# Kernel tuning notes

Hardware: AMD Instinct MI355X
Metric: run time of the kernel (lower is better)

## Reference

```python
import jax, jax.numpy as jnp
import numpy as np

NUM_ANTENNAS = 16
D = 0.5
WAVELENGTH = 1.0
RHO = 0.8


def setup_inputs() -> dict:
    key = jax.random.key(0)
    k = jax.random.split(key, 5)
    return {
        "W": jax.random.normal(k[0], (2_000_000, 2 * NUM_ANTENNAS), dtype=jnp.float32),
        "Hc_real": jax.random.normal(k[1], (4, 8, NUM_ANTENNAS), dtype=jnp.float32),
        "Hc_imag": jax.random.normal(k[2], (4, 8, NUM_ANTENNAS), dtype=jnp.float32),
        "Hs_real": jax.random.normal(k[3], (4, 4, NUM_ANTENNAS), dtype=jnp.float32),
        "Hs_imag": jax.random.normal(k[4], (4, 4, NUM_ANTENNAS), dtype=jnp.float32),
    }


def _estimate_angles(h_real, h_imag):
    """Vectorized version of the per-(b,t) phase-unwrap + OLS slope fit.

    h_real/h_imag: [B, T, N] -> angles [B, T] in degrees.
    """
    n = jnp.arange(NUM_ANTENNAS, dtype=h_real.dtype)
    phases = jnp.arctan2(h_imag, h_real)                      # torch.angle
    pd = jnp.diff(phases, axis=-1)
    pd = (pd + jnp.pi) % (2.0 * jnp.pi) - jnp.pi              # wrap to (-pi, pi]
    zeros = jnp.zeros(phases.shape[:-1] + (1,), phases.dtype)
    unwrapped = jnp.concatenate([zeros, jnp.cumsum(pd, axis=-1)], axis=-1)  # [B,T,N]
    # OLS slope of unwrapped vs n (closed form of solve(XtX, XtY) with X=[n,1])
    n_c = n - n.mean()
    slope = (unwrapped * n_c).sum(-1) / (n_c * n_c).sum()     # [B,T]
    sin_theta = jnp.clip(slope * WAVELENGTH / (2.0 * jnp.pi * D), -1.0, 1.0)
    return -jnp.rad2deg(jnp.arcsin(sin_theta))


def _steering_phase(angles_deg):
    # phase[t, n] = 2*pi*d*n*sin(theta_t)/wavelength  -> [T, N]
    n = jnp.arange(NUM_ANTENNAS, dtype=angles_deg.dtype)
    s = jnp.sin(jnp.deg2rad(angles_deg))
    return 2.0 * jnp.pi * D * s[:, None] * n[None, :] / WAVELENGTH


def reference(W, Hc_real, Hc_imag, Hs_real, Hs_imag):
    user_angles = _estimate_angles(Hc_real, Hc_imag)[0]       # [Tc]
    target_angles = _estimate_angles(Hs_real, Hs_imag)[0]     # [Ts]

    Wr = W[:, :NUM_ANTENNAS]
    Wi = W[:, NUM_ANTENNAS:]

    def gains(phase):  # |w_cplx @ conj(sv).T|, all-real math
        c = jnp.cos(phase)  # [T, N]
        s = jnp.sin(phase)
        re = Wr @ c.T + Wi @ s.T  # [B, T]
        im = Wi @ c.T - Wr @ s.T
        return jnp.sqrt(re * re + im * im)

    user_gains = gains(_steering_phase(user_angles))          # [B, Tc]
    target_gains = gains(_steering_phase(target_angles))      # [B, Ts]

    min_user_gain = user_gains.min(axis=1)
    sum_user_gain = user_gains.sum(axis=1)
    avg_target_gain = target_gains.mean(axis=1)

    comm_loss = -RHO * 2.5 * (min_user_gain + 0.1 * sum_user_gain)
    sens_loss = -(1.0 - RHO) * avg_target_gain
    return jnp.mean(comm_loss + sens_loss)
```

## Files before the change

kernel.cpp:

```cpp
#include <hip/hip_runtime.h>
#include <math.h>

#define NA 16
#define NBEAM 12
#define NUSER 8

#define ACC_OFFSET 1536

__global__ void mtl_angles_kernel(const float* __restrict__ Hc_r, const float* __restrict__ Hc_i,
                                  const float* __restrict__ Hs_r, const float* __restrict__ Hs_i,
                                  float* __restrict__ table, double* __restrict__ acc,
                                  unsigned* __restrict__ done) {
    int t = threadIdx.x;
    if (t == 0) { *acc = 0.0; *done = 0u; }
    if (t >= NBEAM) return;

    const float* re;
    const float* im;
    if (t < NUSER) { re = Hc_r + t * NA;           im = Hc_i + t * NA; }
    else           { re = Hs_r + (t - NUSER) * NA; im = Hs_i + (t - NUSER) * NA; }

    const float PI_F   = 3.14159265358979323846f;
    const float TWO_PI = 6.28318530717958647692f;

    float ph[NA];
    #pragma unroll
    for (int n = 0; n < NA; ++n) ph[n] = atan2f(im[n], re[n]);

    float unw = 0.f, dotsum = 0.f;
    #pragma unroll
    for (int n = 1; n < NA; ++n) {
        float pd = ph[n] - ph[n - 1];
        float x  = pd + PI_F;
        float m  = fmodf(x, TWO_PI);
        if (m < 0.f) m += TWO_PI;
        pd = m - PI_F;
        unw += pd;
        dotsum += unw * ((float)n - 7.5f);
    }
    float slope = dotsum / 340.0f;
    float sin_theta = slope / PI_F;
    sin_theta = fminf(1.0f, fmaxf(-1.0f, sin_theta));
    float st = -sin_theta;

    #pragma unroll
    for (int n = 0; n < NA; ++n) {
        float phase = PI_F * st * (float)n;
        table[t * 2 * NA + n]      = cosf(phase);
        table[t * 2 * NA + NA + n] = sinf(phase);
    }
}

__device__ __forceinline__ float dot4(float4 a, float4 b) {
    return a.x * b.x + a.y * b.y + a.z * b.z + a.w * b.w;
}

__device__ __forceinline__ void load_lds16(const float* g, float* l) {
    __builtin_amdgcn_global_load_lds(
        (const __attribute__((address_space(1))) void*)g,
        (__attribute__((address_space(3))) void*)l, 16, 0, 0);
}

__device__ __forceinline__ float row_loss(const float4* w, const float* tbs) {
    float minU = 3.4e38f, sumU = 0.f, sumT = 0.f;
    #pragma unroll 1
    for (int j = 0; j < NBEAM; ++j) {
        const float4* tc = (const float4*)(tbs + j * 32);
        float re = 0.f, im = 0.f;
        #pragma unroll
        for (int q = 0; q < 4; ++q) {
            float4 c = tc[q], s = tc[q + 4];
            float4 wr = w[q], wi = w[q + 4];
            re += dot4(wr, c) + dot4(wi, s);
            im += dot4(wi, c) - dot4(wr, s);
        }
        float g = sqrtf(re * re + im * im);
        if (j < NUSER) { minU = fminf(minU, g); sumU += g; }
        else           { sumT += g; }
    }
    return -2.0f * (minU + 0.1f * sumU) - 0.05f * sumT;
}

__global__ __launch_bounds__(256, 4) void mtl_gains_kernel(const float* __restrict__ W,
                                                           const float* __restrict__ table,
                                                           double* __restrict__ acc,
                                                           unsigned* __restrict__ done,
                                                           float* __restrict__ out, int rows) {
    __shared__ float sh[4 * 2 * 1024];
    __shared__ float tbs[NBEAM * 2 * NA];
    __shared__ float wsum[4];

    const int t = threadIdx.x;
    for (int i = t; i < NBEAM * 2 * NA; i += blockDim.x) tbs[i] = table[i];
    __syncthreads();

    const int wid  = t >> 6;
    const int lane = t & 63;
    float* buf0 = sh + wid * 2048;
    float* buf1 = buf0 + 1024;

    const int sq      = (lane & 7) ^ ((lane >> 3) & 7);
    const int src_off = (lane >> 3) * 32 + sq * 4;

    const int ntiles = rows >> 5;
    const int nwaves = gridDim.x * 4;
    const int gw     = blockIdx.x * 4 + wid;
    const int cnt    = ntiles / nwaves;
    const int rem    = ntiles % nwaves;
    const int t0     = gw * cnt + (gw < rem ? gw : rem);
    const int t1     = t0 + cnt + (gw < rem ? 1 : 0);

    const int h      = lane >> 5;
    const int row    = lane & 31;
    const int jbase  = h * 6;
    const float* tb  = tbs + jbase * 2 * NA;

    float local = 0.f;

    if (t0 < t1) {
        {
            const float* src = W + (size_t)t0 * 1024 + src_off;
            #pragma unroll
            for (int k = 0; k < 4; ++k) load_lds16(src + k * 256, buf0 + k * 256);
        }
        #pragma unroll 1
        for (int tt = t0; tt < t1; ++tt) {
            float* cur = ((tt - t0) & 1) ? buf1 : buf0;
            float* nxt = ((tt - t0) & 1) ? buf0 : buf1;
            if (tt + 1 < t1) {
                const float* src = W + (size_t)(tt + 1) * 1024 + src_off;
                #pragma unroll
                for (int k = 0; k < 4; ++k) load_lds16(src + k * 256, nxt + k * 256);
                asm volatile("s_waitcnt vmcnt(4)" ::: "memory");
            } else {
                asm volatile("s_waitcnt vmcnt(0)" ::: "memory");
            }

            const float* myrow = cur + row * 32;
            float4 w[8];
            #pragma unroll
            for (int q = 0; q < 8; ++q) {
                int s = q ^ (row & 7);
                w[q] = *(const float4*)(myrow + s * 4);
            }

            float minU = 3.4e38f, sumU = 0.f, sumT = 0.f;
            #pragma unroll 1
            for (int jj = 0; jj < 6; ++jj) {
                const float4* tc = (const float4*)(tb + jj * 32);
                float re = 0.f, im = 0.f;
                #pragma unroll
                for (int q = 0; q < 4; ++q) {
                    float4 c = tc[q], s = tc[q + 4];
                    float4 wr = w[q], wi = w[q + 4];
                    re += dot4(wr, c) + dot4(wi, s);
                    im += dot4(wi, c) - dot4(wr, s);
                }
                float g = sqrtf(re * re + im * im);
                bool isU = (jbase + jj) < NUSER;
                minU = isU ? fminf(minU, g) : minU;
                sumU += isU ? g : 0.f;
                sumT += isU ? 0.f : g;
            }
            minU = fminf(minU, __shfl_xor(minU, 32));
            sumU += __shfl_xor(sumU, 32);
            sumT += __shfl_xor(sumT, 32);
            local += 0.5f * (-2.0f * (minU + 0.1f * sumU) - 0.05f * sumT);
        }
    }

    int tailbase = ntiles << 5;
    if (blockIdx.x == 0) {
        int r = tailbase + t;
        if (r < rows) {
            const float4* wp = (const float4*)(W + (size_t)r * 32);
            float4 w[8];
            #pragma unroll
            for (int i = 0; i < 8; ++i) w[i] = wp[i];
            local += row_loss(w, tbs);
        }
    }

    #pragma unroll
    for (int off = 32; off > 0; off >>= 1) local += __shfl_down(local, off);
    if (lane == 0) wsum[wid] = local;
    __syncthreads();
    if (t == 0) {
        float b = wsum[0] + wsum[1] + wsum[2] + wsum[3];
        atomicAdd(acc, (double)b);
        __threadfence();
        unsigned prev = atomicAdd(done, 1u);
        if (prev == gridDim.x - 1) {
            double total = atomicAdd(acc, 0.0);
            out[0] = (float)(total / (double)rows);
        }
    }
}

extern "C" void kernel_launch(void* const* d_in, const int* in_sizes, int n_in,
                              void* d_out, int out_size, void* d_ws, size_t ws_size,
                              hipStream_t stream) {
    const float* W    = (const float*)d_in[0];
    const float* Hc_r = (const float*)d_in[1];
    const float* Hc_i = (const float*)d_in[2];
    const float* Hs_r = (const float*)d_in[3];
    const float* Hs_i = (const float*)d_in[4];
    float* out = (float*)d_out;

    int rows = in_sizes[0] / (2 * NA);
    float*    table = (float*)d_ws;
    double*   acc   = (double*)((char*)d_ws + ACC_OFFSET);
    unsigned* done  = (unsigned*)((char*)d_ws + ACC_OFFSET + 8);

    mtl_angles_kernel<<<1, 64, 0, stream>>>(Hc_r, Hc_i, Hs_r, Hs_i, table, acc, done);

    mtl_gains_kernel<<<1024, 256, 0, stream>>>(W, table, acc, done, out, rows);
}
```

Baseline: 408.4 us.

## Replace last-block completion counter with separate finalize kernel and split beam loops

Removes the threadfence and done-counter atomic that let the last block compute the final mean, and launches a tiny finalize kernel instead. The per-row beam loop is split into a user loop and a target loop so the per-iteration user/target select logic disappears. Launch bounds are expressed through an explicit waves-per-EU attribute. The extra kernel launch adds a small fixed cost in exchange for less per-block synchronisation.

```diff
diff --git a/kernel.cpp b/kernel.cpp
--- a/kernel.cpp
+++ b/kernel.cpp
@@ -9,10 +9,9 @@
 
 __global__ void mtl_angles_kernel(const float* __restrict__ Hc_r, const float* __restrict__ Hc_i,
                                   const float* __restrict__ Hs_r, const float* __restrict__ Hs_i,
-                                  float* __restrict__ table, double* __restrict__ acc,
-                                  unsigned* __restrict__ done) {
+                                  float* __restrict__ table, double* __restrict__ acc) {
     int t = threadIdx.x;
-    if (t == 0) { *acc = 0.0; *done = 0u; }
+    if (t == 0) *acc = 0.0;
     if (t >= NBEAM) return;
 
     const float* re;
@@ -61,31 +60,35 @@
         (__attribute__((address_space(3))) void*)l, 16, 0, 0);
 }
 
+__device__ __forceinline__ float beam_gain(const float4* w, const float* trow) {
+    const float4* tc = (const float4*)trow;
+    float re = 0.f, im = 0.f;
+    #pragma unroll
+    for (int q = 0; q < 4; ++q) {
+        float4 c = tc[q], s = tc[q + 4];
+        float4 wr = w[q], wi = w[q + 4];
+        re += dot4(wr, c) + dot4(wi, s);
+        im += dot4(wi, c) - dot4(wr, s);
+    }
+    return sqrtf(re * re + im * im);
+}
+
 __device__ __forceinline__ float row_loss(const float4* w, const float* tbs) {
     float minU = 3.4e38f, sumU = 0.f, sumT = 0.f;
     #pragma unroll 1
     for (int j = 0; j < NBEAM; ++j) {
-        const float4* tc = (const float4*)(tbs + j * 32);
-        float re = 0.f, im = 0.f;
-        #pragma unroll
-        for (int q = 0; q < 4; ++q) {
-            float4 c = tc[q], s = tc[q + 4];
-            float4 wr = w[q], wi = w[q + 4];
-            re += dot4(wr, c) + dot4(wi, s);
-            im += dot4(wi, c) - dot4(wr, s);
-        }
-        float g = sqrtf(re * re + im * im);
+        float g = beam_gain(w, tbs + j * 32);
         if (j < NUSER) { minU = fminf(minU, g); sumU += g; }
         else           { sumT += g; }
     }
     return -2.0f * (minU + 0.1f * sumU) - 0.05f * sumT;
 }
 
-__global__ __launch_bounds__(256, 4) void mtl_gains_kernel(const float* __restrict__ W,
-                                                           const float* __restrict__ table,
-                                                           double* __restrict__ acc,
-                                                           unsigned* __restrict__ done,
-                                                           float* __restrict__ out, int rows) {
+__global__ __launch_bounds__(256)
+__attribute__((amdgpu_waves_per_eu(4, 4)))
+void mtl_gains_kernel(const float* __restrict__ W,
+                      const float* __restrict__ table,
+                      double* __restrict__ acc, int rows) {
     __shared__ float sh[4 * 2 * 1024];
     __shared__ float tbs[NBEAM * 2 * NA];
     __shared__ float wsum[4];
@@ -112,8 +115,8 @@
 
     const int h      = lane >> 5;
     const int row    = lane & 31;
-    const int jbase  = h * 6;
-    const float* tb  = tbs + jbase * 2 * NA;
+    const float* tbU = tbs + h * 4 * 32;
+    const float* tbT = tbs + (8 + h * 2) * 32;
 
     float local = 0.f;
 
@@ -146,21 +149,14 @@
 
             float minU = 3.4e38f, sumU = 0.f, sumT = 0.f;
             #pragma unroll 1
-            for (int jj = 0; jj < 6; ++jj) {
-                const float4* tc = (const float4*)(tb + jj * 32);
-                float re = 0.f, im = 0.f;
-                #pragma unroll
-                for (int q = 0; q < 4; ++q) {
-                    float4 c = tc[q], s = tc[q + 4];
-                    float4 wr = w[q], wi = w[q + 4];
-                    re += dot4(wr, c) + dot4(wi, s);
-                    im += dot4(wi, c) - dot4(wr, s);
-                }
-                float g = sqrtf(re * re + im * im);
-                bool isU = (jbase + jj) < NUSER;
-                minU = isU ? fminf(minU, g) : minU;
-                sumU += isU ? g : 0.f;
-                sumT += isU ? 0.f : g;
+            for (int jj = 0; jj < 4; ++jj) {
+                float g = beam_gain(w, tbU + jj * 32);
+                minU = fminf(minU, g);
+                sumU += g;
+            }
+            #pragma unroll 1
+            for (int jj = 0; jj < 2; ++jj) {
+                sumT += beam_gain(w, tbT + jj * 32);
             }
             minU = fminf(minU, __shfl_xor(minU, 32));
             sumU += __shfl_xor(sumU, 32);
@@ -188,13 +184,11 @@
     if (t == 0) {
         float b = wsum[0] + wsum[1] + wsum[2] + wsum[3];
         atomicAdd(acc, (double)b);
-        __threadfence();
-        unsigned prev = atomicAdd(done, 1u);
-        if (prev == gridDim.x - 1) {
-            double total = atomicAdd(acc, 0.0);
-            out[0] = (float)(total / (double)rows);
-        }
-    }
+    }
+}
+
+__global__ void mtl_finalize_kernel(const double* __restrict__ acc, float* __restrict__ out, int rows) {
+    if (threadIdx.x == 0) out[0] = (float)(*acc / (double)rows);
 }
 
 extern "C" void kernel_launch(void* const* d_in, const int* in_sizes, int n_in,
@@ -208,11 +202,12 @@
     float* out = (float*)d_out;
 
     int rows = in_sizes[0] / (2 * NA);
-    float*    table = (float*)d_ws;
-    double*   acc   = (double*)((char*)d_ws + ACC_OFFSET);
-    unsigned* done  = (unsigned*)((char*)d_ws + ACC_OFFSET + 8);
-
-    mtl_angles_kernel<<<1, 64, 0, stream>>>(Hc_r, Hc_i, Hs_r, Hs_i, table, acc, done);
-
-    mtl_gains_kernel<<<1024, 256, 0, stream>>>(W, table, acc, done, out, rows);
-}
+    float*  table = (float*)d_ws;
+    double* acc   = (double*)((char*)d_ws + ACC_OFFSET);
+
+    mtl_angles_kernel<<<1, 64, 0, stream>>>(Hc_r, Hc_i, Hs_r, Hs_i, table, acc);
+
+    mtl_gains_kernel<<<1024, 256, 0, stream>>>(W, table, acc, rows);
+
+    mtl_finalize_kernel<<<1, 64, 0, stream>>>(acc, out, rows);
+}
```

New measurement: 375.9 us. -8.0%, faster.
